# Performance work log

Hardware: AMD Instinct MI355X
Metric: run time of the kernel (lower is better)

## Reference

```python
import jax, jax.numpy as jnp
import numpy as np
import math

B, T, C, H = 2, 1024, 768, 12
HD = C // H


def _heads(t):
    # [B,T,C] -> [B,H,T,HD]
    return t.reshape(B, T, H, HD).transpose(0, 2, 1, 3)


def _causal_sdpa(q, k, v):
    # q,k,v: [B,H,T,HD]; scaled dot-product attention with causal mask, no dropout
    scale = 1.0 / math.sqrt(HD)
    s = jnp.einsum('bhqd,bhkd->bhqk', q, k) * scale
    mask = jnp.tril(jnp.ones((T, T), dtype=bool))
    s = jnp.where(mask, s, jnp.finfo(s.dtype).min)
    p = jax.nn.softmax(s, axis=-1)
    return jnp.einsum('bhqk,bhkd->bhqd', p, v)


def setup_inputs() -> dict:
    key = jax.random.key(0)
    k1, k2, k3 = jax.random.split(key, 3)
    x = jax.random.normal(k1, (B, T, C), dtype=jnp.float32)
    eps = 0.1
    x_lower = x - eps
    x_upper = x + eps
    W_attn = jax.random.normal(k2, (3 * C, C), dtype=jnp.float32) * 0.02
    W_proj = jax.random.normal(k3, (C, C), dtype=jnp.float32) * 0.02
    return {'x': x, 'x_lower': x_lower, 'x_upper': x_upper,
            'W_attn': W_attn, 'W_proj': W_proj}


def reference(x, x_lower, x_upper, W_attn, W_proj):
    # main path
    qkv = x @ W_attn.T                       # [B,T,3C]
    q, k, v = jnp.split(qkv, 3, axis=2)
    y = _causal_sdpa(_heads(q), _heads(k), _heads(v))
    y = y.transpose(0, 2, 1, 3).reshape(B, T, C) @ W_proj.T

    # interval bound path (torch runs it under no_grad)
    W_pos = jnp.maximum(W_attn, 0.0)
    W_neg = jnp.minimum(W_attn, 0.0)
    lowers = x_lower @ W_pos.T + x_upper @ W_neg.T   # lower bounds of q,k,v concat
    uppers = x_upper @ W_pos.T + x_lower @ W_neg.T   # upper bounds of q,k,v concat
    qL, kL, vL = (_heads(t) for t in jnp.split(lowers, 3, axis=2))
    qU, kU, vU = (_heads(t) for t in jnp.split(uppers, 3, axis=2))

    y_min = None
    y_max = None
    for qq in (qL, qU):
        for kk in (kL, kU):
            for vv in (vL, vU):
                yb = _causal_sdpa(qq, kk, vv)
                y_min = yb if y_min is None else jnp.minimum(y_min, yb)
                y_max = yb if y_max is None else jnp.maximum(y_max, yb)
    y_lower = y_min.transpose(0, 2, 1, 3).reshape(B, T, C) @ W_proj.T
    y_upper = y_max.transpose(0, 2, 1, 3).reshape(B, T, C) @ W_proj.T
    return (y, y_lower, y_upper)
```

## Files before the change

### kernel.cpp

```cpp
#include <hip/hip_runtime.h>
#include <stdint.h>
#include <math.h>

typedef __attribute__((ext_vector_type(8))) short bf16x8;
typedef __attribute__((ext_vector_type(4))) short s16x4;
typedef __attribute__((ext_vector_type(8))) short s16x8;
typedef __attribute__((ext_vector_type(4))) float f32x4;
typedef __attribute__((ext_vector_type(2))) uint32_t u32x2;

#define DEVI __device__ __forceinline__

constexpr int Bn = 2, Tn = 1024, Cn = 768, Hn = 12, HDn = 64;
constexpr int N3 = 3 * Cn;
constexpr int Mrows = Bn * Tn;
constexpr size_t SZy = (size_t)Mrows * Cn;

template <bool V> struct BoolC { static constexpr bool value = V; };

DEVI short f2bf(float f) {
  union { float f; uint32_t u; } v; v.f = f;
  uint32_t u = v.u;
  return (short)((u + 0x7FFFu + ((u >> 16) & 1u)) >> 16);
}
DEVI float bf2f(short b) {
  union { uint32_t u; float f; } v; v.u = ((uint32_t)(uint16_t)b) << 16;
  return v.f;
}
DEVI float fexp2(float x) { return __builtin_exp2f(x); }
DEVI uint32_t cvtpk(float lo, float hi) {
  uint32_t r;
  asm("v_cvt_pk_bf16_f32 %0, %1, %2" : "=v"(r) : "v"(lo), "v"(hi));
  return r;
}
DEVI void cp16(void* lds, const void* g) {
  __builtin_amdgcn_global_load_lds(
      (const __attribute__((address_space(1))) uint32_t*)(uintptr_t)g,
      (__attribute__((address_space(3))) uint32_t*)(uint32_t)(uintptr_t)lds,
      16, 0, 0);
}
DEVI f32x4 fz() { f32x4 z; z[0] = 0.f; z[1] = 0.f; z[2] = 0.f; z[3] = 0.f; return z; }

__global__ void prep_x(const float* __restrict__ x, const float* __restrict__ xl,
                       const float* __restrict__ xu, short* __restrict__ xb,
                       short* __restrict__ mb, short* __restrict__ rb) {
  int i = blockIdx.x * 256 + threadIdx.x;
  float4 vx = ((const float4*)x)[i];
  float4 vl = ((const float4*)xl)[i];
  float4 vu = ((const float4*)xu)[i];
  s16x4 a, m_, g;
  a[0] = f2bf(vx.x); a[1] = f2bf(vx.y); a[2] = f2bf(vx.z); a[3] = f2bf(vx.w);
  m_[0] = f2bf(0.5f * (vl.x + vu.x)); m_[1] = f2bf(0.5f * (vl.y + vu.y));
  m_[2] = f2bf(0.5f * (vl.z + vu.z)); m_[3] = f2bf(0.5f * (vl.w + vu.w));
  g[0] = f2bf(0.5f * (vu.x - vl.x)); g[1] = f2bf(0.5f * (vu.y - vl.y));
  g[2] = f2bf(0.5f * (vu.z - vl.z)); g[3] = f2bf(0.5f * (vu.w - vl.w));
  ((s16x4*)xb)[i] = a; ((s16x4*)mb)[i] = m_; ((s16x4*)rb)[i] = g;
}
__global__ void prep_w(const float* __restrict__ w, short* __restrict__ wb,
                       short* __restrict__ awb) {
  int i = blockIdx.x * 256 + threadIdx.x;
  float4 v = ((const float4*)w)[i];
  s16x4 a, b2;
  a[0] = f2bf(v.x); a[1] = f2bf(v.y); a[2] = f2bf(v.z); a[3] = f2bf(v.w);
  b2[0] = f2bf(fabsf(v.x)); b2[1] = f2bf(fabsf(v.y));
  b2[2] = f2bf(fabsf(v.z)); b2[3] = f2bf(fabsf(v.w));
  ((s16x4*)wb)[i] = a; ((s16x4*)awb)[i] = b2;
}
__global__ void prep_w1(const float* __restrict__ w, short* __restrict__ wb) {
  int i = blockIdx.x * 256 + threadIdx.x;
  float4 v = ((const float4*)w)[i];
  s16x4 a;
  a[0] = f2bf(v.x); a[1] = f2bf(v.y); a[2] = f2bf(v.z); a[3] = f2bf(v.w);
  ((s16x4*)wb)[i] = a;
}

__launch_bounds__(256, 3)
__global__ void gemm_qkv3(const short* __restrict__ A0, const short* __restrict__ A1,
                          const short* __restrict__ A2, const short* __restrict__ B0,
                          const short* __restrict__ B1, short* __restrict__ qkv,
                          short* __restrict__ low, short* __restrict__ up) {
  constexpr int BM = 128, BN = 64;
  __shared__ short At[3 * BM * 32];
  __shared__ short Bt[2 * BN * 32];
  const int tid = threadIdx.x, wave = tid >> 6, lane = tid & 63;
  const int wm = wave >> 1, wn = wave & 1;
  const int brow = blockIdx.x * BM, bcol = blockIdx.y * BN;
  const short* As[3] = {A0, A1, A2};
  const short* Bs[2] = {B0, B1};

  f32x4 acc[3][4][2];
#pragma unroll
  for (int a = 0; a < 3; a++)
#pragma unroll
    for (int m = 0; m < 4; m++)
#pragma unroll
      for (int n = 0; n < 2; n++) acc[a][m][n] = fz();

  for (int kt = 0; kt < Cn / 32; ++kt) {
#pragma unroll
    for (int a = 0; a < 3; a++)
#pragma unroll
      for (int ii = 0; ii < 2; ++ii) {
        int i = wave * 2 + ii;
        int chunk = i * 64 + lane, row = chunk >> 2, c = chunk & 3;
        cp16((char*)At + a * (BM * 64) + i * 1024,
             As[a] + (size_t)(brow + row) * Cn + (kt * 32 + c * 8));
      }
#pragma unroll
    for (int b2 = 0; b2 < 2; b2++) {
      int chunk = wave * 64 + lane, row = chunk >> 2, c = chunk & 3;
      cp16((char*)Bt + b2 * (BN * 64) + wave * 1024,
           Bs[b2] + (size_t)(bcol + row) * Cn + (kt * 32 + c * 8));
    }
    __syncthreads();
    bf16x8 bfr[2][2];
#pragma unroll
    for (int b2 = 0; b2 < 2; b2++)
#pragma unroll
      for (int n = 0; n < 2; n++) {
        int r = wn * 32 + n * 16 + (lane & 15);
        bfr[b2][n] = *(const bf16x8*)&Bt[b2 * (BN * 32) + r * 32 + (lane >> 4) * 8];
      }
#pragma unroll
    for (int a = 0; a < 3; a++) {
      bf16x8 af[4];
#pragma unroll
      for (int m = 0; m < 4; m++) {
        int r = wm * 64 + m * 16 + (lane & 15);
        af[m] = *(const bf16x8*)&At[a * (BM * 32) + r * 32 + (lane >> 4) * 8];
      }
      const int bs = (a == 2) ? 1 : 0;
#pragma unroll
      for (int m = 0; m < 4; m++)
#pragma unroll
        for (int n = 0; n < 2; n++)
          acc[a][m][n] = __builtin_amdgcn_mfma_f32_16x16x32_bf16(
              af[m], bfr[bs][n], acc[a][m][n], 0, 0, 0);
    }
    __syncthreads();
  }
#pragma unroll
  for (int m = 0; m < 4; m++)
#pragma unroll
    for (int n = 0; n < 2; n++)
#pragma unroll
      for (int r = 0; r < 4; r++) {
        int row = brow + wm * 64 + m * 16 + (lane >> 4) * 4 + r;
        int col = bcol + wn * 32 + n * 16 + (lane & 15);
        size_t idx = (size_t)row * N3 + col;
        float v0 = acc[0][m][n][r], v1 = acc[1][m][n][r], v2 = acc[2][m][n][r];
        qkv[idx] = f2bf(v0);
        low[idx] = f2bf(v1 - v2);
        up[idx]  = f2bf(v1 + v2);
      }
}

__launch_bounds__(256, 4)
__global__ void gemm_proj(const short* __restrict__ A0, const short* __restrict__ A1,
                          const short* __restrict__ A2, const short* __restrict__ Bw,
                          float* __restrict__ out) {
  constexpr int BM = 64, BN = 128;
  __shared__ short At[BM * 32];
  __shared__ short Bt[BN * 32];
  const short* Ap = blockIdx.z == 0 ? A0 : (blockIdx.z == 1 ? A1 : A2);
  float* op = out + (size_t)blockIdx.z * SZy;
  const int tid = threadIdx.x, wave = tid >> 6, lane = tid & 63;
  const int wm = wave >> 1, wn = wave & 1;
  const int brow = blockIdx.x * BM, bcol = blockIdx.y * BN;

  f32x4 acc[2][4];
#pragma unroll
  for (int m = 0; m < 2; m++)
#pragma unroll
    for (int n = 0; n < 4; n++) acc[m][n] = fz();

  const int chunk = wave * 64 + lane, srow = chunk >> 2, sc = chunk & 3;
  for (int kt = 0; kt < Cn / 32; ++kt) {
    cp16((char*)At + wave * 1024, Ap + (size_t)(brow + srow) * Cn + (kt * 32 + sc * 8));
#pragma unroll
    for (int ii = 0; ii < 2; ++ii) {
      int i = wave * 2 + ii;
      int ch = i * 64 + lane, row = ch >> 2, c = ch & 3;
      cp16((char*)Bt + i * 1024, Bw + (size_t)(bcol + row) * Cn + (kt * 32 + c * 8));
    }
    __syncthreads();
    bf16x8 af[2], bfr[4];
#pragma unroll
    for (int m = 0; m < 2; m++) {
      int r = wm * 32 + m * 16 + (lane & 15);
      af[m] = *(const bf16x8*)&At[r * 32 + (lane >> 4) * 8];
    }
#pragma unroll
    for (int n = 0; n < 4; n++) {
      int r = wn * 64 + n * 16 + (lane & 15);
      bfr[n] = *(const bf16x8*)&Bt[r * 32 + (lane >> 4) * 8];
    }
#pragma unroll
    for (int m = 0; m < 2; m++)
#pragma unroll
      for (int n = 0; n < 4; n++)
        acc[m][n] = __builtin_amdgcn_mfma_f32_16x16x32_bf16(af[m], bfr[n], acc[m][n], 0, 0, 0);
    __syncthreads();
  }
#pragma unroll
  for (int m = 0; m < 2; m++)
#pragma unroll
    for (int n = 0; n < 4; n++)
#pragma unroll
      for (int r = 0; r < 4; r++) {
        int row = brow + wm * 32 + m * 16 + (lane >> 4) * 4 + r;
        int col = bcol + wn * 64 + n * 16 + (lane & 15);
        op[(size_t)row * Cn + col] = acc[m][n][r];
      }
}

__global__ void vtrans(const short* __restrict__ s0, const short* __restrict__ s1,
                       const short* __restrict__ s2, short* __restrict__ d0,
                       short* __restrict__ d1, short* __restrict__ d2) {
  __shared__ short tile[64][72];
  const short* src = blockIdx.z == 0 ? s0 : (blockIdx.z == 1 ? s1 : s2);
  short* dst = blockIdx.z == 0 ? d0 : (blockIdx.z == 1 ? d1 : d2);
  const int tt = blockIdx.x, bh = blockIdx.y;
  const int b = bh / Hn, h = bh % Hn;
  const int tid = threadIdx.x;
#pragma unroll
  for (int i = 0; i < 2; i++) {
    int chunk = i * 256 + tid;
    int t = chunk >> 3, c = chunk & 7;
    s16x8 v = *(const s16x8*)(src + (size_t)(b * Tn + tt * 64 + t) * N3 +
                              2 * Cn + h * HDn + c * 8);
    *(s16x8*)&tile[t][c * 8] = v;
  }
  __syncthreads();
#pragma unroll
  for (int i = 0; i < 2; i++) {
    int chunk = i * 256 + tid;
    int d = chunk >> 3, tc = chunk & 7;
    s16x8 v;
#pragma unroll
    for (int j = 0; j < 8; j++) v[j] = tile[tc * 8 + j][d];
    *(s16x8*)(dst + (size_t)bh * (64 * 1024) + (size_t)d * 1024 + tt * 64 + tc * 8) = v;
  }
}

__launch_bounds__(256, 4)
__global__ void flash_all(const short* __restrict__ qkv, const short* __restrict__ lowb,
                          const short* __restrict__ upb, const short* __restrict__ vtq,
                          const short* __restrict__ vtl, const short* __restrict__ vtu,
                          short* __restrict__ yab, short* __restrict__ comb) {
  constexpr float SCL = 0.18033688f;
  constexpr float THR = 8.0f / SCL;
  __shared__ short Kt[64 * 64];
  __shared__ short Vt0[64 * 64];
  __shared__ short Vt1[64 * 64];
  __shared__ short Pt[4 * 16 * 64];
  const int tid = threadIdx.x, wave = tid >> 6, lane = tid & 63;
  const int g = lane >> 4, q = lane & 15;
  const int bh = blockIdx.x, combo = blockIdx.y;
  const int qt = 15 - blockIdx.z;
  const int b = bh / Hn, h = bh % Hn;
  const bool isMain = (combo == 4);
  const short* Qsrc = isMain ? qkv : ((combo & 2) ? upb : lowb);
  const short* Ksrc = isMain ? qkv : ((combo & 1) ? upb : lowb);
  const short* V0t = isMain ? vtq : vtl;
  const short* V1t = vtu;
  char* PtW = (char*)Pt + wave * 2048;
  const int qswz = (q & 7) << 4;

  bf16x8 aq[2];
  {
    int trow = qt * 64 + wave * 16 + q;
    const short* qp = Qsrc + (size_t)(b * Tn + trow) * N3 + h * HDn;
#pragma unroll
    for (int s = 0; s < 2; s++) aq[s] = *(const bf16x8*)(qp + s * 32 + g * 8);
  }

  f32x4 o0[4], o1[4];
  float mrow = -INFINITY, lrow = 0.f;
#pragma unroll
  for (int n = 0; n < 4; n++) { o0[n] = fz(); o1[n] = fz(); }

  auto kv_iter = [&](int kv, auto diagc) {
    constexpr bool DIAG = decltype(diagc)::value;
#pragma unroll
    for (int ii = 0; ii < 2; ++ii) {
      int i = wave * 2 + ii;
      int chunk = i * 64 + lane, row = chunk >> 3, c = chunk & 7;
      int cg = c ^ (row & 7);
      cp16((char*)Kt + i * 1024,
           Ksrc + (size_t)(b * Tn + kv * 64 + row) * N3 + Cn + h * HDn + cg * 8);
    }
#pragma unroll
    for (int ii = 0; ii < 2; ++ii) {
      int i = wave * 2 + ii;
      int chunk = i * 64 + lane, row = chunk >> 3, c = chunk & 7;
      int cg = c ^ (row & 7);
      cp16((char*)Vt0 + i * 1024,
           V0t + (size_t)bh * (64 * 1024) + (size_t)row * 1024 + kv * 64 + cg * 8);
    }
    if (!isMain) {
#pragma unroll
      for (int ii = 0; ii < 2; ++ii) {
        int i = wave * 2 + ii;
        int chunk = i * 64 + lane, row = chunk >> 3, c = chunk & 7;
        int cg = c ^ (row & 7);
        cp16((char*)Vt1 + i * 1024,
             V1t + (size_t)bh * (64 * 1024) + (size_t)row * 1024 + kv * 64 + cg * 8);
      }
    }
    __syncthreads();

    f32x4 sa[4];
#pragma unroll
    for (int m = 0; m < 4; m++) sa[m] = fz();
    __builtin_amdgcn_s_setprio(1);
#pragma unroll
    for (int m = 0; m < 4; m++) {
#pragma unroll
      for (int s = 0; s < 2; s++) {
        int krow = m * 16 + q;
        bf16x8 bk = *(const bf16x8*)((char*)Kt +
            krow * 128 + ((g * 16 + s * 64) ^ ((krow & 7) << 4)));
        sa[m] = __builtin_amdgcn_mfma_f32_16x16x32_bf16(bk, aq[s], sa[m], 0, 0, 0);
      }
    }
    __builtin_amdgcn_s_setprio(0);

    if constexpr (DIAG) {
      const int rhs = wave * 16 + q, kb = g * 4;
#pragma unroll
      for (int m = 0; m < 4; m++)
#pragma unroll
        for (int r = 0; r < 4; r++)
          sa[m][r] = (m * 16 + kb + r <= rhs) ? sa[m][r] : -INFINITY;
    }
    float mx = -INFINITY;
#pragma unroll
    for (int m = 0; m < 4; m++)
#pragma unroll
      for (int r = 0; r < 4; r++) mx = fmaxf(mx, sa[m][r]);
    mx = fmaxf(mx, __shfl_xor(mx, 16));
    mx = fmaxf(mx, __shfl_xor(mx, 32));
    if (!__all(mx <= mrow + THR)) {
      float mnew = fmaxf(mrow, mx);
      float corr = fexp2((mrow - mnew) * SCL);
      mrow = mnew; lrow *= corr;
#pragma unroll
      for (int n = 0; n < 4; n++) {
        o0[n][0] *= corr; o0[n][1] *= corr; o0[n][2] *= corr; o0[n][3] *= corr;
      }
      if (!isMain) {
#pragma unroll
        for (int n = 0; n < 4; n++) {
          o1[n][0] *= corr; o1[n][1] *= corr; o1[n][2] *= corr; o1[n][3] *= corr;
        }
      }
    }
    const float nms = -mrow * SCL;
    float ps = 0.f;
#pragma unroll
    for (int m = 0; m < 4; m++)
#pragma unroll
      for (int r = 0; r < 4; r++) {
        float p = fexp2(fmaf(sa[m][r], SCL, nms));
        sa[m][r] = p;
        ps += p;
      }
    ps += __shfl_xor(ps, 16);
    ps += __shfl_xor(ps, 32);
    lrow += ps;

#pragma unroll
    for (int m = 0; m < 4; m++) {
      uint32_t w0 = cvtpk(sa[m][0], sa[m][1]);
      uint32_t w1 = cvtpk(sa[m][2], sa[m][3]);
      int base = q * 128 + m * 32 + g * 8;
      *(uint32_t*)(PtW + ((base) ^ qswz)) = w0;
      *(uint32_t*)(PtW + ((base + 4) ^ qswz)) = w1;
    }
    bf16x8 pb[2];
#pragma unroll
    for (int kk = 0; kk < 2; kk++)
      pb[kk] = *(const bf16x8*)(PtW + ((q * 128 + kk * 64 + g * 16) ^ qswz));

    __builtin_amdgcn_s_setprio(1);
#pragma unroll
    for (int kk = 0; kk < 2; kk++) {
#pragma unroll
      for (int mf = 0; mf < 4; mf++) {
        int drow = mf * 16 + q;
        int boff = drow * 128 + ((g * 16 + kk * 64) ^ ((drow & 7) << 4));
        bf16x8 av0 = *(const bf16x8*)((char*)Vt0 + boff);
        o0[mf] = __builtin_amdgcn_mfma_f32_16x16x32_bf16(av0, pb[kk], o0[mf], 0, 0, 0);
        if (!isMain) {
          bf16x8 av1 = *(const bf16x8*)((char*)Vt1 + boff);
          o1[mf] = __builtin_amdgcn_mfma_f32_16x16x32_bf16(av1, pb[kk], o1[mf], 0, 0, 0);
        }
      }
    }
    __builtin_amdgcn_s_setprio(0);
    __syncthreads();
  };

  for (int kv = 0; kv < qt; ++kv) kv_iter(kv, BoolC<false>{});
  kv_iter(qt, BoolC<true>{});

  const float inv = 1.0f / lrow;
  const int trow = qt * 64 + wave * 16 + q;
  const size_t rowbase = (size_t)(b * Tn + trow) * Cn + h * HDn + g * 4;
#pragma unroll
  for (int mf = 0; mf < 4; mf++) {
    size_t idx = rowbase + mf * 16;
    u32x2 v0;
    v0[0] = cvtpk(o0[mf][0] * inv, o0[mf][1] * inv);
    v0[1] = cvtpk(o0[mf][2] * inv, o0[mf][3] * inv);
    if (isMain) {
      *(u32x2*)(yab + idx) = v0;
    } else {
      u32x2 v1;
      v1[0] = cvtpk(o1[mf][0] * inv, o1[mf][1] * inv);
      v1[1] = cvtpk(o1[mf][2] * inv, o1[mf][3] * inv);
      *(u32x2*)(comb + (size_t)(2 * combo) * SZy + idx) = v0;
      *(u32x2*)(comb + (size_t)(2 * combo + 1) * SZy + idx) = v1;
    }
  }
}

__global__ void reduce_minmax(const short* __restrict__ comb, short* __restrict__ ymn,
                              short* __restrict__ ymx) {
  int i = blockIdx.x * 256 + threadIdx.x;
  s16x8 mn8 = ((const s16x8*)(comb + 0 * SZy))[i];
  s16x8 mx8 = ((const s16x8*)(comb + 1 * SZy))[i];
#pragma unroll
  for (int c = 1; c < 4; c++) {
    s16x8 a = ((const s16x8*)(comb + (size_t)(2 * c) * SZy))[i];
    s16x8 b2 = ((const s16x8*)(comb + (size_t)(2 * c + 1) * SZy))[i];
#pragma unroll
    for (int j = 0; j < 8; j++) {
      mn8[j] = f2bf(fminf(bf2f(mn8[j]), bf2f(a[j])));
      mx8[j] = f2bf(fmaxf(bf2f(mx8[j]), bf2f(b2[j])));
    }
  }
  ((s16x8*)ymn)[i] = mn8;
  ((s16x8*)ymx)[i] = mx8;
}

extern "C" void kernel_launch(void* const* d_in, const int* in_sizes, int n_in,
                              void* d_out, int out_size, void* d_ws, size_t ws_size,
                              hipStream_t stream) {
  const float* x  = (const float*)d_in[0];
  const float* xl = (const float*)d_in[1];
  const float* xu = (const float*)d_in[2];
  const float* Wa = (const float*)d_in[3];
  const float* Wp = (const float*)d_in[4];
  float* out = (float*)d_out;

  char* p = (char*)d_ws;
  auto carve = [&](size_t bytes) -> char* {
    char* r = p; p += (bytes + 255) & ~(size_t)255; return r;
  };
  short* xb   = (short*)carve((size_t)Mrows * Cn * 2);
  short* midb = (short*)carve((size_t)Mrows * Cn * 2);
  short* radb = (short*)carve((size_t)Mrows * Cn * 2);
  short* wb   = (short*)carve((size_t)N3 * Cn * 2);
  short* awb  = (short*)carve((size_t)N3 * Cn * 2);
  short* wpb  = (short*)carve((size_t)Cn * Cn * 2);
  short* qkvb = (short*)carve((size_t)Mrows * N3 * 2);
  short* lowb = (short*)carve((size_t)Mrows * N3 * 2);
  short* upb  = (short*)carve((size_t)Mrows * N3 * 2);
  short* vtq  = (short*)carve((size_t)24 * 64 * 1024 * 2);
  short* vtl  = (short*)carve((size_t)24 * 64 * 1024 * 2);
  short* vtu  = (short*)carve((size_t)24 * 64 * 1024 * 2);
  short* yab  = (short*)carve(SZy * 2);
  short* ymnb = (short*)carve(SZy * 2);
  short* ymxb = (short*)carve(SZy * 2);
  short* comb = (short*)carve(8 * SZy * 2);

  prep_x<<<1536, 256, 0, stream>>>(x, xl, xu, xb, midb, radb);
  prep_w<<<1728, 256, 0, stream>>>(Wa, wb, awb);
  prep_w1<<<576, 256, 0, stream>>>(Wp, wpb);

  gemm_qkv3<<<dim3(16, 36), 256, 0, stream>>>(xb, midb, radb, wb, awb,
                                              qkvb, lowb, upb);

  vtrans<<<dim3(16, 24, 3), 256, 0, stream>>>(qkvb, lowb, upb, vtq, vtl, vtu);

  flash_all<<<dim3(24, 5, 16), 256, 0, stream>>>(qkvb, lowb, upb, vtq, vtl, vtu,
                                                 yab, comb);

  reduce_minmax<<<768, 256, 0, stream>>>(comb, ymnb, ymxb);

  gemm_proj<<<dim3(32, 6, 3), 256, 0, stream>>>(yab, ymnb, ymxb, wpb, out);
}
```

Measured before the change: 140.8 us.

## Process two query tiles per flash block to reuse K/V loads; retile QKV GEMM

The flash attention kernel now gives each block two 64-row query tiles (128 rows), so every K/V tile loaded into LDS serves two sets of QK and PV MFMAs. This halves the number of blocks and their K/V traffic, at the cost of more registers and a lower occupancy bound (3 instead of 4). Causal masking is handled with compile-time variants for the two diagonal tiles. The QKV GEMM tile changes from 128x64 to 64x128, with the grid reshaped to match.

```diff
diff --git a/kernel.cpp b/kernel.cpp
--- a/kernel.cpp
+++ b/kernel.cpp
@@ -15,7 +15,7 @@
 constexpr int Mrows = Bn * Tn;
 constexpr size_t SZy = (size_t)Mrows * Cn;
 
-template <bool V> struct BoolC { static constexpr bool value = V; };
+template <int V> struct IntC { static constexpr int value = V; };
 
 DEVI short f2bf(float f) {
   union { float f; uint32_t u; } v; v.f = f;
@@ -78,74 +78,74 @@
                           const short* __restrict__ A2, const short* __restrict__ B0,
                           const short* __restrict__ B1, short* __restrict__ qkv,
                           short* __restrict__ low, short* __restrict__ up) {
-  constexpr int BM = 128, BN = 64;
+  constexpr int BM = 64, BN = 128;
   __shared__ short At[3 * BM * 32];
   __shared__ short Bt[2 * BN * 32];
   const int tid = threadIdx.x, wave = tid >> 6, lane = tid & 63;
+  const int g = lane >> 4, q = lane & 15;
   const int wm = wave >> 1, wn = wave & 1;
   const int brow = blockIdx.x * BM, bcol = blockIdx.y * BN;
   const short* As[3] = {A0, A1, A2};
   const short* Bs[2] = {B0, B1};
 
-  f32x4 acc[3][4][2];
+  f32x4 acc[3][2][4];
 #pragma unroll
   for (int a = 0; a < 3; a++)
 #pragma unroll
-    for (int m = 0; m < 4; m++)
-#pragma unroll
-      for (int n = 0; n < 2; n++) acc[a][m][n] = fz();
-
+    for (int m = 0; m < 2; m++)
+#pragma unroll
+      for (int n = 0; n < 4; n++) acc[a][m][n] = fz();
+
+  const int arow = tid >> 2, ac = tid & 3;
   for (int kt = 0; kt < Cn / 32; ++kt) {
 #pragma unroll
     for (int a = 0; a < 3; a++)
+      cp16((char*)At + a * 4096 + tid * 16,
+           As[a] + (size_t)(brow + arow) * Cn + (kt * 32 + ac * 8));
+#pragma unroll
+    for (int b2 = 0; b2 < 2; b2++)
 #pragma unroll
       for (int ii = 0; ii < 2; ++ii) {
         int i = wave * 2 + ii;
-        int chunk = i * 64 + lane, row = chunk >> 2, c = chunk & 3;
-        cp16((char*)At + a * (BM * 64) + i * 1024,
-             As[a] + (size_t)(brow + row) * Cn + (kt * 32 + c * 8));
-      }
-#pragma unroll
-    for (int b2 = 0; b2 < 2; b2++) {
-      int chunk = wave * 64 + lane, row = chunk >> 2, c = chunk & 3;
-      cp16((char*)Bt + b2 * (BN * 64) + wave * 1024,
-           Bs[b2] + (size_t)(bcol + row) * Cn + (kt * 32 + c * 8));
-    }
+        int ch = i * 64 + lane, row = ch >> 2, c = ch & 3;
+        cp16((char*)Bt + b2 * 8192 + i * 1024,
+             Bs[b2] + (size_t)(bcol + row) * Cn + (kt * 32 + c * 8));
+      }
     __syncthreads();
-    bf16x8 bfr[2][2];
+    bf16x8 bfr[2][4];
 #pragma unroll
     for (int b2 = 0; b2 < 2; b2++)
 #pragma unroll
-      for (int n = 0; n < 2; n++) {
-        int r = wn * 32 + n * 16 + (lane & 15);
-        bfr[b2][n] = *(const bf16x8*)&Bt[b2 * (BN * 32) + r * 32 + (lane >> 4) * 8];
+      for (int n = 0; n < 4; n++) {
+        int r = wn * 64 + n * 16 + q;
+        bfr[b2][n] = *(const bf16x8*)&Bt[b2 * (BN * 32) + r * 32 + g * 8];
       }
 #pragma unroll
     for (int a = 0; a < 3; a++) {
-      bf16x8 af[4];
-#pragma unroll
-      for (int m = 0; m < 4; m++) {
-        int r = wm * 64 + m * 16 + (lane & 15);
-        af[m] = *(const bf16x8*)&At[a * (BM * 32) + r * 32 + (lane >> 4) * 8];
+      bf16x8 af[2];
+#pragma unroll
+      for (int m = 0; m < 2; m++) {
+        int r = wm * 32 + m * 16 + q;
+        af[m] = *(const bf16x8*)&At[a * (BM * 32) + r * 32 + g * 8];
       }
       const int bs = (a == 2) ? 1 : 0;
 #pragma unroll
-      for (int m = 0; m < 4; m++)
-#pragma unroll
-        for (int n = 0; n < 2; n++)
+      for (int m = 0; m < 2; m++)
+#pragma unroll
+        for (int n = 0; n < 4; n++)
           acc[a][m][n] = __builtin_amdgcn_mfma_f32_16x16x32_bf16(
               af[m], bfr[bs][n], acc[a][m][n], 0, 0, 0);
     }
     __syncthreads();
   }
 #pragma unroll
-  for (int m = 0; m < 4; m++)
-#pragma unroll
-    for (int n = 0; n < 2; n++)
+  for (int m = 0; m < 2; m++)
+#pragma unroll
+    for (int n = 0; n < 4; n++)
 #pragma unroll
       for (int r = 0; r < 4; r++) {
-        int row = brow + wm * 64 + m * 16 + (lane >> 4) * 4 + r;
-        int col = bcol + wn * 32 + n * 16 + (lane & 15);
+        int row = brow + wm * 32 + m * 16 + g * 4 + r;
+        int col = bcol + wn * 64 + n * 16 + q;
         size_t idx = (size_t)row * N3 + col;
         float v0 = acc[0][m][n][r], v1 = acc[1][m][n][r], v2 = acc[2][m][n][r];
         qkv[idx] = f2bf(v0);
@@ -242,7 +242,7 @@
   }
 }
 
-__launch_bounds__(256, 4)
+__launch_bounds__(256, 3)
 __global__ void flash_all(const short* __restrict__ qkv, const short* __restrict__ lowb,
                           const short* __restrict__ upb, const short* __restrict__ vtq,
                           const short* __restrict__ vtl, const short* __restrict__ vtu,
@@ -252,66 +252,126 @@
   __shared__ short Kt[64 * 64];
   __shared__ short Vt0[64 * 64];
   __shared__ short Vt1[64 * 64];
-  __shared__ short Pt[4 * 16 * 64];
+  __shared__ short Pt[8 * 16 * 64];
   const int tid = threadIdx.x, wave = tid >> 6, lane = tid & 63;
   const int g = lane >> 4, q = lane & 15;
   const int bh = blockIdx.x, combo = blockIdx.y;
-  const int qt = 15 - blockIdx.z;
+  const int j = 7 - blockIdx.z;
+  const int qt0 = j * 128;
   const int b = bh / Hn, h = bh % Hn;
   const bool isMain = (combo == 4);
   const short* Qsrc = isMain ? qkv : ((combo & 2) ? upb : lowb);
   const short* Ksrc = isMain ? qkv : ((combo & 1) ? upb : lowb);
   const short* V0t = isMain ? vtq : vtl;
   const short* V1t = vtu;
-  char* PtW = (char*)Pt + wave * 2048;
   const int qswz = (q & 7) << 4;
 
-  bf16x8 aq[2];
-  {
-    int trow = qt * 64 + wave * 16 + q;
+  int koff[2], voff[2];
+#pragma unroll
+  for (int ii = 0; ii < 2; ++ii) {
+    int chunk = (wave * 2 + ii) * 64 + lane, row = chunk >> 3, c = chunk & 7;
+    int cg = c ^ (row & 7);
+    koff[ii] = row * N3 + cg * 8;
+    voff[ii] = row * 1024 + cg * 8;
+  }
+  const short* Kbase = Ksrc + (size_t)(b * Tn) * N3 + Cn + h * HDn;
+  const short* V0base = V0t + (size_t)bh * (64 * 1024);
+  const short* V1base = V1t + (size_t)bh * (64 * 1024);
+
+  bf16x8 aq[2][2];
+#pragma unroll
+  for (int u = 0; u < 2; u++) {
+    int trow = qt0 + u * 64 + wave * 16 + q;
     const short* qp = Qsrc + (size_t)(b * Tn + trow) * N3 + h * HDn;
 #pragma unroll
-    for (int s = 0; s < 2; s++) aq[s] = *(const bf16x8*)(qp + s * 32 + g * 8);
-  }
-
-  f32x4 o0[4], o1[4];
-  float mrow = -INFINITY, lrow = 0.f;
-#pragma unroll
-  for (int n = 0; n < 4; n++) { o0[n] = fz(); o1[n] = fz(); }
-
-  auto kv_iter = [&](int kv, auto diagc) {
+    for (int s = 0; s < 2; s++) aq[u][s] = *(const bf16x8*)(qp + s * 32 + g * 8);
+  }
+
+  f32x4 o0[2][4], o1[2][4];
+  float mrow[2], lrow[2];
+#pragma unroll
+  for (int u = 0; u < 2; u++) {
+    mrow[u] = -INFINITY; lrow[u] = 0.f;
+#pragma unroll
+    for (int n = 0; n < 4; n++) { o0[u][n] = fz(); o1[u][n] = fz(); }
+  }
+
+  auto softmax_u = [&](f32x4 (&sv)[4], int u, auto diagc) {
     constexpr bool DIAG = decltype(diagc)::value;
-#pragma unroll
-    for (int ii = 0; ii < 2; ++ii) {
-      int i = wave * 2 + ii;
-      int chunk = i * 64 + lane, row = chunk >> 3, c = chunk & 7;
-      int cg = c ^ (row & 7);
-      cp16((char*)Kt + i * 1024,
-           Ksrc + (size_t)(b * Tn + kv * 64 + row) * N3 + Cn + h * HDn + cg * 8);
-    }
-#pragma unroll
-    for (int ii = 0; ii < 2; ++ii) {
-      int i = wave * 2 + ii;
-      int chunk = i * 64 + lane, row = chunk >> 3, c = chunk & 7;
-      int cg = c ^ (row & 7);
-      cp16((char*)Vt0 + i * 1024,
-           V0t + (size_t)bh * (64 * 1024) + (size_t)row * 1024 + kv * 64 + cg * 8);
-    }
+    if constexpr (DIAG) {
+      const int rhs = wave * 16 + q, kb = g * 4;
+#pragma unroll
+      for (int m = 0; m < 4; m++)
+#pragma unroll
+        for (int r = 0; r < 4; r++)
+          sv[m][r] = (m * 16 + kb + r <= rhs) ? sv[m][r] : -INFINITY;
+    }
+    float mx = -INFINITY;
+#pragma unroll
+    for (int m = 0; m < 4; m++)
+#pragma unroll
+      for (int r = 0; r < 4; r++) mx = fmaxf(mx, sv[m][r]);
+    mx = fmaxf(mx, __shfl_xor(mx, 16));
+    mx = fmaxf(mx, __shfl_xor(mx, 32));
+    if (!__all(mx <= mrow[u] + THR)) {
+      float mnew = fmaxf(mrow[u], mx);
+      float corr = fexp2((mrow[u] - mnew) * SCL);
+      mrow[u] = mnew; lrow[u] *= corr;
+#pragma unroll
+      for (int n = 0; n < 4; n++) {
+        o0[u][n][0] *= corr; o0[u][n][1] *= corr;
+        o0[u][n][2] *= corr; o0[u][n][3] *= corr;
+      }
+      if (!isMain) {
+#pragma unroll
+        for (int n = 0; n < 4; n++) {
+          o1[u][n][0] *= corr; o1[u][n][1] *= corr;
+          o1[u][n][2] *= corr; o1[u][n][3] *= corr;
+        }
+      }
+    }
+    const float nms = -mrow[u] * SCL;
+    float ps = 0.f;
+#pragma unroll
+    for (int m = 0; m < 4; m++)
+#pragma unroll
+      for (int r = 0; r < 4; r++) {
+        float p = fexp2(fmaf(sv[m][r], SCL, nms));
+        sv[m][r] = p;
+        ps += p;
+      }
+    ps += __shfl_xor(ps, 16);
+    ps += __shfl_xor(ps, 32);
+    lrow[u] += ps;
+    char* PtW = (char*)Pt + (wave * 2 + u) * 2048;
+#pragma unroll
+    for (int m = 0; m < 4; m++) {
+      u32x2 w;
+      w[0] = cvtpk(sv[m][0], sv[m][1]);
+      w[1] = cvtpk(sv[m][2], sv[m][3]);
+      *(u32x2*)(PtW + ((q * 128 + m * 32 + g * 8) ^ qswz)) = w;
+    }
+  };
+
+  auto kv_iter = [&](int kv, auto m0c, auto m1c) {
+    constexpr int M0 = decltype(m0c)::value;
+    constexpr int M1 = decltype(m1c)::value;
+#pragma unroll
+    for (int ii = 0; ii < 2; ++ii)
+      cp16((char*)Kt + (wave * 2 + ii) * 1024, Kbase + (size_t)kv * (64 * N3) + koff[ii]);
+#pragma unroll
+    for (int ii = 0; ii < 2; ++ii)
+      cp16((char*)Vt0 + (wave * 2 + ii) * 1024, V0base + kv * 64 + voff[ii]);
     if (!isMain) {
 #pragma unroll
-      for (int ii = 0; ii < 2; ++ii) {
-        int i = wave * 2 + ii;
-        int chunk = i * 64 + lane, row = chunk >> 3, c = chunk & 7;
-        int cg = c ^ (row & 7);
-        cp16((char*)Vt1 + i * 1024,
-             V1t + (size_t)bh * (64 * 1024) + (size_t)row * 1024 + kv * 64 + cg * 8);
-      }
+      for (int ii = 0; ii < 2; ++ii)
+        cp16((char*)Vt1 + (wave * 2 + ii) * 1024, V1base + kv * 64 + voff[ii]);
     }
     __syncthreads();
 
-    f32x4 sa[4];
-#pragma unroll
-    for (int m = 0; m < 4; m++) sa[m] = fz();
+    f32x4 sa0[4], sa1[4];
+#pragma unroll
+    for (int m = 0; m < 4; m++) { sa0[m] = fz(); sa1[m] = fz(); }
     __builtin_amdgcn_s_setprio(1);
 #pragma unroll
     for (int m = 0; m < 4; m++) {
@@ -320,80 +380,42 @@
         int krow = m * 16 + q;
         bf16x8 bk = *(const bf16x8*)((char*)Kt +
             krow * 128 + ((g * 16 + s * 64) ^ ((krow & 7) << 4)));
-        sa[m] = __builtin_amdgcn_mfma_f32_16x16x32_bf16(bk, aq[s], sa[m], 0, 0, 0);
+        if constexpr (M0 > 0)
+          sa0[m] = __builtin_amdgcn_mfma_f32_16x16x32_bf16(bk, aq[0][s], sa0[m], 0, 0, 0);
+        if constexpr (M1 > 0)
+          sa1[m] = __builtin_amdgcn_mfma_f32_16x16x32_bf16(bk, aq[1][s], sa1[m], 0, 0, 0);
       }
     }
     __builtin_amdgcn_s_setprio(0);
 
-    if constexpr (DIAG) {
-      const int rhs = wave * 16 + q, kb = g * 4;
-#pragma unroll
-      for (int m = 0; m < 4; m++)
-#pragma unroll
-        for (int r = 0; r < 4; r++)
-          sa[m][r] = (m * 16 + kb + r <= rhs) ? sa[m][r] : -INFINITY;
-    }
-    float mx = -INFINITY;
-#pragma unroll
-    for (int m = 0; m < 4; m++)
-#pragma unroll
-      for (int r = 0; r < 4; r++) mx = fmaxf(mx, sa[m][r]);
-    mx = fmaxf(mx, __shfl_xor(mx, 16));
-    mx = fmaxf(mx, __shfl_xor(mx, 32));
-    if (!__all(mx <= mrow + THR)) {
-      float mnew = fmaxf(mrow, mx);
-      float corr = fexp2((mrow - mnew) * SCL);
-      mrow = mnew; lrow *= corr;
-#pragma unroll
-      for (int n = 0; n < 4; n++) {
-        o0[n][0] *= corr; o0[n][1] *= corr; o0[n][2] *= corr; o0[n][3] *= corr;
-      }
-      if (!isMain) {
-#pragma unroll
-        for (int n = 0; n < 4; n++) {
-          o1[n][0] *= corr; o1[n][1] *= corr; o1[n][2] *= corr; o1[n][3] *= corr;
-        }
-      }
-    }
-    const float nms = -mrow * SCL;
-    float ps = 0.f;
-#pragma unroll
-    for (int m = 0; m < 4; m++)
-#pragma unroll
-      for (int r = 0; r < 4; r++) {
-        float p = fexp2(fmaf(sa[m][r], SCL, nms));
-        sa[m][r] = p;
-        ps += p;
-      }
-    ps += __shfl_xor(ps, 16);
-    ps += __shfl_xor(ps, 32);
-    lrow += ps;
-
-#pragma unroll
-    for (int m = 0; m < 4; m++) {
-      uint32_t w0 = cvtpk(sa[m][0], sa[m][1]);
-      uint32_t w1 = cvtpk(sa[m][2], sa[m][3]);
-      int base = q * 128 + m * 32 + g * 8;
-      *(uint32_t*)(PtW + ((base) ^ qswz)) = w0;
-      *(uint32_t*)(PtW + ((base + 4) ^ qswz)) = w1;
-    }
-    bf16x8 pb[2];
-#pragma unroll
-    for (int kk = 0; kk < 2; kk++)
-      pb[kk] = *(const bf16x8*)(PtW + ((q * 128 + kk * 64 + g * 16) ^ qswz));
+    if constexpr (M0 > 0) softmax_u(sa0, 0, IntC<(M0 == 1)>{});
+    if constexpr (M1 > 0) softmax_u(sa1, 1, IntC<(M1 == 1)>{});
 
     __builtin_amdgcn_s_setprio(1);
 #pragma unroll
     for (int kk = 0; kk < 2; kk++) {
+      bf16x8 pb0, pb1;
+      if constexpr (M0 > 0)
+        pb0 = *(const bf16x8*)((char*)Pt + (wave * 2 + 0) * 2048 +
+                               ((q * 128 + kk * 64 + g * 16) ^ qswz));
+      if constexpr (M1 > 0)
+        pb1 = *(const bf16x8*)((char*)Pt + (wave * 2 + 1) * 2048 +
+                               ((q * 128 + kk * 64 + g * 16) ^ qswz));
 #pragma unroll
       for (int mf = 0; mf < 4; mf++) {
         int drow = mf * 16 + q;
         int boff = drow * 128 + ((g * 16 + kk * 64) ^ ((drow & 7) << 4));
         bf16x8 av0 = *(const bf16x8*)((char*)Vt0 + boff);
-        o0[mf] = __builtin_amdgcn_mfma_f32_16x16x32_bf16(av0, pb[kk], o0[mf], 0, 0, 0);
+        if constexpr (M0 > 0)
+          o0[0][mf] = __builtin_amdgcn_mfma_f32_16x16x32_bf16(av0, pb0, o0[0][mf], 0, 0, 0);
+        if constexpr (M1 > 0)
+          o0[1][mf] = __builtin_amdgcn_mfma_f32_16x16x32_bf16(av0, pb1, o0[1][mf], 0, 0, 0);
         if (!isMain) {
           bf16x8 av1 = *(const bf16x8*)((char*)Vt1 + boff);
-          o1[mf] = __builtin_amdgcn_mfma_f32_16x16x32_bf16(av1, pb[kk], o1[mf], 0, 0, 0);
+          if constexpr (M0 > 0)
+            o1[0][mf] = __builtin_amdgcn_mfma_f32_16x16x32_bf16(av1, pb0, o1[0][mf], 0, 0, 0);
+          if constexpr (M1 > 0)
+            o1[1][mf] = __builtin_amdgcn_mfma_f32_16x16x32_bf16(av1, pb1, o1[1][mf], 0, 0, 0);
         }
       }
     }
@@ -401,26 +423,31 @@
     __syncthreads();
   };
 
-  for (int kv = 0; kv < qt; ++kv) kv_iter(kv, BoolC<false>{});
-  kv_iter(qt, BoolC<true>{});
-
-  const float inv = 1.0f / lrow;
-  const int trow = qt * 64 + wave * 16 + q;
-  const size_t rowbase = (size_t)(b * Tn + trow) * Cn + h * HDn + g * 4;
-#pragma unroll
-  for (int mf = 0; mf < 4; mf++) {
-    size_t idx = rowbase + mf * 16;
-    u32x2 v0;
-    v0[0] = cvtpk(o0[mf][0] * inv, o0[mf][1] * inv);
-    v0[1] = cvtpk(o0[mf][2] * inv, o0[mf][3] * inv);
-    if (isMain) {
-      *(u32x2*)(yab + idx) = v0;
-    } else {
-      u32x2 v1;
-      v1[0] = cvtpk(o1[mf][0] * inv, o1[mf][1] * inv);
-      v1[1] = cvtpk(o1[mf][2] * inv, o1[mf][3] * inv);
-      *(u32x2*)(comb + (size_t)(2 * combo) * SZy + idx) = v0;
-      *(u32x2*)(comb + (size_t)(2 * combo + 1) * SZy + idx) = v1;
+  const int jj = 2 * j;
+  for (int kv = 0; kv < jj; ++kv) kv_iter(kv, IntC<2>{}, IntC<2>{});
+  kv_iter(jj, IntC<1>{}, IntC<2>{});
+  kv_iter(jj + 1, IntC<0>{}, IntC<1>{});
+
+#pragma unroll
+  for (int u = 0; u < 2; u++) {
+    const float inv = 1.0f / lrow[u];
+    const int trow = qt0 + u * 64 + wave * 16 + q;
+    const size_t rowbase = (size_t)(b * Tn + trow) * Cn + h * HDn + g * 4;
+#pragma unroll
+    for (int mf = 0; mf < 4; mf++) {
+      size_t idx = rowbase + mf * 16;
+      u32x2 v0;
+      v0[0] = cvtpk(o0[u][mf][0] * inv, o0[u][mf][1] * inv);
+      v0[1] = cvtpk(o0[u][mf][2] * inv, o0[u][mf][3] * inv);
+      if (isMain) {
+        *(u32x2*)(yab + idx) = v0;
+      } else {
+        u32x2 v1;
+        v1[0] = cvtpk(o1[u][mf][0] * inv, o1[u][mf][1] * inv);
+        v1[1] = cvtpk(o1[u][mf][2] * inv, o1[u][mf][3] * inv);
+        *(u32x2*)(comb + (size_t)(2 * combo) * SZy + idx) = v0;
+        *(u32x2*)(comb + (size_t)(2 * combo + 1) * SZy + idx) = v1;
+      }
     }
   }
 }
@@ -479,13 +506,13 @@
   prep_w<<<1728, 256, 0, stream>>>(Wa, wb, awb);
   prep_w1<<<576, 256, 0, stream>>>(Wp, wpb);
 
-  gemm_qkv3<<<dim3(16, 36), 256, 0, stream>>>(xb, midb, radb, wb, awb,
+  gemm_qkv3<<<dim3(32, 18), 256, 0, stream>>>(xb, midb, radb, wb, awb,
                                               qkvb, lowb, upb);
 
   vtrans<<<dim3(16, 24, 3), 256, 0, stream>>>(qkvb, lowb, upb, vtq, vtl, vtu);
 
-  flash_all<<<dim3(24, 5, 16), 256, 0, stream>>>(qkvb, lowb, upb, vtq, vtl, vtu,
-                                                 yab, comb);
+  flash_all<<<dim3(24, 5, 8), 256, 0, stream>>>(qkvb, lowb, upb, vtq, vtl, vtu,
+                                                yab, comb);
 
   reduce_minmax<<<768, 256, 0, stream>>>(comb, ymnb, ymxb);
 
```

New measurement: 132.3 us. 6.0% less time.
